# Kernel optimization log

Hardware: AMD Instinct MI355X
Metric: run time of the kernel (lower is better)

## Reference

```python
import jax, jax.numpy as jnp
import numpy as np

GROUP_SIZE = 128

def setup_inputs() -> dict:
    key = jax.random.key(0)
    k1, k2, k3 = jax.random.split(key, 3)
    B, S, K, N = 4, 128, 4096, 11008
    num_groups = K // GROUP_SIZE
    x = jax.random.normal(k1, (B, S, K), dtype=jnp.float16)
    # packed int4 weights: each byte holds two nibbles (low = even k, high = odd k)
    weight_packed = jax.random.randint(k2, (N, K // 2), 0, 256, dtype=jnp.int32)
    scales = (jax.random.uniform(k3, (N, num_groups), dtype=jnp.float16) * jnp.float16(0.1))
    return {"x": x, "weight_packed": weight_packed, "scales": scales}

def reference(x, weight_packed, scales):
    # x: (B, S, K) fp16; weight_packed: (N, K//2) int in [0,256); scales: (N, K//group_size) fp16
    N, Kp = weight_packed.shape
    K = Kp * 2
    # Unpack nibbles: even k -> low nibble, odd k -> high nibble (interleaved along K)
    low = weight_packed & 0x0F
    high = (weight_packed >> 4) & 0x0F
    w_int = jnp.stack([low, high], axis=-1).reshape(N, K).astype(jnp.float32)  # (N, K)
    # Per-group dequantization: w = scale * (q - 8)
    scale_full = jnp.repeat(scales.astype(jnp.float32), GROUP_SIZE, axis=1)    # (N, K)
    w = scale_full * (w_int - 8.0)
    # fp32 accumulation, fp16 output (matches kernel: float accum, half store)
    y = jnp.einsum('bsk,nk->bsn', x.astype(jnp.float32), w)
    return y.astype(jnp.float16)
```

## Files before the change

### kernel.cpp

```cpp
#include <hip/hip_runtime.h>


typedef __attribute__((ext_vector_type(8)))  short short8;
typedef __attribute__((ext_vector_type(16))) float f32x16;
typedef __attribute__((ext_vector_type(4)))  float f32x4;
typedef __attribute__((ext_vector_type(4)))  int   i32x4;
typedef __attribute__((ext_vector_type(2)))  int   i32x2;

#define M_DIM 512
#define N_DIM 11008
#define K_DIM 4096
#define BM 256
#define BN 128
#define BK 64
#define KSPLIT 4
#define PAD 8
#define THREADS 256
#define NTILE_M (M_DIM / BM)
#define NTILE_N (N_DIM / BN)
#define NTILES  (NTILE_M * NTILE_N)
#define TILE_ELEMS (BM * BN)

#if defined(__has_builtin)
#  if __has_builtin(__builtin_amdgcn_cvt_pk_bf16_f32)
#    define HAVE_PK_BF16 1
#  endif
#endif
#ifndef HAVE_PK_BF16
#  define HAVE_PK_BF16 0
#endif

__device__ __forceinline__ unsigned int fbits(float f) {
    union { float f; unsigned int u; } c; c.f = f; return c.u;
}
__device__ __forceinline__ int pack2bf(float lo, float hi) {
#if HAVE_PK_BF16
    typedef __attribute__((ext_vector_type(2))) __bf16 bf16x2;
    bf16x2 p = __builtin_amdgcn_cvt_pk_bf16_f32(lo, hi);
    int r; __builtin_memcpy(&r, &p, 4);
    return r;
#else
    unsigned int ul = fbits(lo), uh = fbits(hi);
    unsigned int l = (ul + 0x7FFFu + ((ul >> 16) & 1u)) >> 16;
    unsigned int h = (uh + 0x7FFFu + ((uh >> 16) & 1u)) & 0xFFFF0000u;
    return (int)(h | l);
#endif
}

__global__ __launch_bounds__(THREADS)
void cvt_x(const float* __restrict__ x, unsigned short* __restrict__ xw)
{
    int idx = (blockIdx.x * THREADS + threadIdx.x) * 4;
    f32x4 v = *(const f32x4*)(x + idx);
    i32x2 p;
    p[0] = pack2bf(v[0], v[1]);
    p[1] = pack2bf(v[2], v[3]);
    *(i32x2*)(xw + idx) = p;
}

template<int KS, bool PRECVT>
__global__ __launch_bounds__(THREADS, 2)
void dq_gemm(const unsigned short* __restrict__ xw,
             const float* __restrict__ xf,
             const int* __restrict__ wp,
             const float* __restrict__ scales,
             float* __restrict__ out,
             float* __restrict__ partials)
{
    __shared__ __align__(16) unsigned short sA[BM][BK + PAD];
    __shared__ __align__(16) unsigned short sB[BN][BK + PAD];

    const int t  = threadIdx.x;
    const int bx = blockIdx.x;

    int m_idx, nb, ksp;
    if (KS == 4) {
        m_idx = (bx >> 3) & 1;
        int rest = (bx & 7) | ((bx >> 4) << 3);
        ksp = rest & 3;
        nb  = rest >> 2;
    } else {
        m_idx = bx & 1;
        nb  = bx >> 1;
        ksp = 0;
    }
    const int m0 = m_idx * BM;
    const int n0 = nb * BN;
    const int k0 = ksp * (K_DIM / KS);
    const int KITERS = (K_DIM / KS) / BK;

    const int wave = t >> 6;
    const int lane = t & 63;
    const int wm = (wave & 1) * 128;
    const int wn = (wave >> 1) * 64;
    const int lr = lane & 31;
    const int lk = (lane >> 5) * 8;

    f32x16 acc[4][2] = {};

    for (int kk = 0; kk < KITERS; ++kk) {
        const int kb = k0 + kk * BK;
        const int g  = kb >> 7;

        if constexpr (PRECVT) {
            #pragma unroll
            for (int i = 0; i < 8; ++i) {
                int c = i * 256 + t, row = c >> 3, col = (c & 7) * 8;
                *(i32x4*)&sA[row][col] =
                    *(const i32x4*)(xw + (size_t)(m0 + row) * K_DIM + kb + col);
            }
        } else {
            #pragma unroll
            for (int i = 0; i < 16; ++i) {
                int c = i * 256 + t, row = c >> 4, col = (c & 15) * 4;
                f32x4 v = *(const f32x4*)(xf + (size_t)(m0 + row) * K_DIM + kb + col);
                i32x2 p;
                p[0] = pack2bf(v[0], v[1]);
                p[1] = pack2bf(v[2], v[3]);
                *(i32x2*)&sA[row][col] = p;
            }
        }

        #pragma unroll
        for (int i = 0; i < 4; ++i) {
            int c = i * 256 + t, row = c >> 3, ic = (c & 7) * 4;
            i32x4 pv = *(const i32x4*)(wp + (size_t)(n0 + row) * (K_DIM / 2) + (kb >> 1) + ic);
            float s  = scales[(size_t)(n0 + row) * (K_DIM / 128) + g];
            float ns8 = s * -8.0f;
            i32x4 res;
            #pragma unroll
            for (int e = 0; e < 4; ++e) {
                int b = pv[e];
                res[e] = pack2bf((float)(b & 15) * s + ns8,
                                 (float)((b >> 4) & 15) * s + ns8);
            }
            *(i32x4*)&sB[row][ic * 2] = res;
        }

        __syncthreads();

        #pragma unroll
        for (int ks = 0; ks < BK; ks += 16) {
            short8 a[4], b[2];
            #pragma unroll
            for (int i = 0; i < 4; ++i)
                a[i] = *(const short8*)&sA[wm + i * 32 + lr][ks + lk];
            #pragma unroll
            for (int j = 0; j < 2; ++j)
                b[j] = *(const short8*)&sB[wn + j * 32 + lr][ks + lk];
            #pragma unroll
            for (int i = 0; i < 4; ++i)
                #pragma unroll
                for (int j = 0; j < 2; ++j)
                    acc[i][j] = __builtin_amdgcn_mfma_f32_32x32x16_bf16(
                        a[i], b[j], acc[i][j], 0, 0, 0);
        }

        __syncthreads();
    }

    const int rbase = (lane >> 5) * 4;
    if constexpr (KS == 1) {
        #pragma unroll
        for (int i = 0; i < 4; ++i) {
            int mg0 = m0 + wm + i * 32 + rbase;
            #pragma unroll
            for (int j = 0; j < 2; ++j) {
                int ng = n0 + wn + j * 32 + lr;
                #pragma unroll
                for (int r = 0; r < 16; ++r)
                    out[(size_t)(mg0 + (r & 3) + 8 * (r >> 2)) * N_DIM + ng] = acc[i][j][r];
            }
        }
    } else {
        float* my = partials + ((size_t)(m_idx * NTILE_N + nb) * KS + ksp) * TILE_ELEMS;
        #pragma unroll
        for (int i = 0; i < 4; ++i)
            #pragma unroll
            for (int j = 0; j < 2; ++j)
                #pragma unroll
                for (int q = 0; q < 4; ++q) {
                    int c = (i * 2 + j) * 4 + q;
                    f32x4 v;
                    v[0] = acc[i][j][q * 4 + 0];
                    v[1] = acc[i][j][q * 4 + 1];
                    v[2] = acc[i][j][q * 4 + 2];
                    v[3] = acc[i][j][q * 4 + 3];
                    *(f32x4*)(my + c * 1024 + t * 4) = v;
                }
    }
}

__global__ __launch_bounds__(THREADS)
void reduce_k(const float* __restrict__ partials, float* __restrict__ out)
{
    __shared__ float sT[128][132];

    const int b    = blockIdx.x;
    const int tile = b >> 1;
    const int h    = b & 1;
    const int m_idx = tile / NTILE_N;
    const int nb    = tile % NTILE_N;
    const int m0 = m_idx * BM + h * 128;
    const int n0 = nb * BN;
    const int u  = threadIdx.x;

    const float* base = partials + (size_t)tile * KSPLIT * TILE_ELEMS;

    #pragma unroll
    for (int it = 0; it < 16; ++it) {
        int idx = it * 256 + u;
        int c   = idx >> 7;
        int tl  = idx & 127;
        int t   = (tl & 63) | (h << 6) | ((tl & 64) << 1);
        int off = c * 1024 + t * 4;
        f32x4 s = *(const f32x4*)(base + off);
        s += *(const f32x4*)(base + TILE_ELEMS + off);
        s += *(const f32x4*)(base + 2 * TILE_ELEMS + off);
        s += *(const f32x4*)(base + 3 * TILE_ELEMS + off);
        int i = c >> 3, j = (c >> 2) & 1, q = c & 3;
        int lane = t & 63, wave = t >> 6;
        int mrow = i * 32 + (lane >> 5) * 4 + 8 * q;
        int ncol = (wave >> 1) * 64 + j * 32 + (lane & 31);
        sT[mrow + 0][ncol] = s[0];
        sT[mrow + 1][ncol] = s[1];
        sT[mrow + 2][ncol] = s[2];
        sT[mrow + 3][ncol] = s[3];
    }
    __syncthreads();

    #pragma unroll
    for (int it = 0; it < 16; ++it) {
        int idx = it * 256 + u;
        int row = idx >> 5;
        int c4  = (idx & 31) * 4;
        f32x4 v = *(const f32x4*)&sT[row][c4];
        *(f32x4*)(out + (size_t)(m0 + row) * N_DIM + n0 + c4) = v;
    }
}

extern "C" void kernel_launch(void* const* d_in, const int* in_sizes, int n_in,
                              void* d_out, int out_size, void* d_ws, size_t ws_size,
                              hipStream_t stream) {
    (void)in_sizes; (void)n_in; (void)out_size;
    const float* x      = (const float*)d_in[0];
    const int*   wpck   = (const int*)d_in[1];
    const float* scales = (const float*)d_in[2];
    float*       out    = (float*)d_out;

    const size_t XW_BYTES   = (size_t)M_DIM * K_DIM * 2;
    const size_t PART_OFF   = XW_BYTES;
    const size_t PART_BYTES = (size_t)NTILES * KSPLIT * TILE_ELEMS * 4;

    if (ws_size >= PART_OFF + PART_BYTES) {
        unsigned short* xw  = (unsigned short*)d_ws;
        float* part = (float*)((char*)d_ws + PART_OFF);
        cvt_x<<<(M_DIM * K_DIM) / (THREADS * 4), THREADS, 0, stream>>>(x, xw);
        dq_gemm<KSPLIT, true><<<NTILES * KSPLIT, THREADS, 0, stream>>>(
            xw, x, wpck, scales, out, part);
        reduce_k<<<NTILES * 2, THREADS, 0, stream>>>(part, out);
    } else if (ws_size >= XW_BYTES) {
        unsigned short* xw = (unsigned short*)d_ws;
        cvt_x<<<(M_DIM * K_DIM) / (THREADS * 4), THREADS, 0, stream>>>(x, xw);
        dq_gemm<1, true><<<NTILES, THREADS, 0, stream>>>(
            xw, x, wpck, scales, out, nullptr);
    } else {
        dq_gemm<1, false><<<NTILES, THREADS, 0, stream>>>(
            nullptr, x, wpck, scales, out, nullptr);
    }
}
```

Measured before the change: 221.1 us.

## Pre-dequantize weights to bf16 and run plain bf16 GEMM with async LDS loads

Replaces the split-K fused dequant GEMM plus reduction with three steps: a separate kernel that dequantizes the whole int4 weight matrix into a bf16 workspace, then a plain bf16 GEMM over 128x128 tiles using 16x16x32 MFMA, XOR-swizzled shared memory, and global_load_lds direct-to-LDS copies. The aim is to take dequant arithmetic out of the GEMM inner loop and drop the partials write/read and the reduction kernel. In exchange it writes and reads back about 90 MB of bf16 weights instead of reading packed int4 directly, and it depends on the workspace being large enough. The GEMM has no double buffering, so loads and MFMA are not overlapped.

```diff
diff --git a/kernel.cpp b/kernel.cpp
--- a/kernel.cpp
+++ b/kernel.cpp
@@ -2,32 +2,33 @@
 
 
 typedef __attribute__((ext_vector_type(8)))  short short8;
-typedef __attribute__((ext_vector_type(16))) float f32x16;
 typedef __attribute__((ext_vector_type(4)))  float f32x4;
 typedef __attribute__((ext_vector_type(4)))  int   i32x4;
 typedef __attribute__((ext_vector_type(2)))  int   i32x2;
+typedef unsigned int   u32;
+typedef unsigned short u16;
 
 #define M_DIM 512
 #define N_DIM 11008
 #define K_DIM 4096
-#define BM 256
+#define BM 128
 #define BN 128
 #define BK 64
-#define KSPLIT 4
-#define PAD 8
 #define THREADS 256
-#define NTILE_M (M_DIM / BM)
-#define NTILE_N (N_DIM / BN)
-#define NTILES  (NTILE_M * NTILE_N)
-#define TILE_ELEMS (BM * BN)
 
 #if defined(__has_builtin)
 #  if __has_builtin(__builtin_amdgcn_cvt_pk_bf16_f32)
 #    define HAVE_PK_BF16 1
 #  endif
+#  if __has_builtin(__builtin_amdgcn_global_load_lds)
+#    define HAVE_GLLDS 1
+#  endif
 #endif
 #ifndef HAVE_PK_BF16
 #  define HAVE_PK_BF16 0
+#endif
+#ifndef HAVE_GLLDS
+#  define HAVE_GLLDS 0
 #endif
 
 __device__ __forceinline__ unsigned int fbits(float f) {
@@ -47,8 +48,16 @@
 #endif
 }
 
+__device__ __forceinline__ void async16(const u16* g, u16* lds_wave_base) {
+#if HAVE_GLLDS
+    __builtin_amdgcn_global_load_lds(
+        (const __attribute__((address_space(1))) u32*)g,
+        (__attribute__((address_space(3))) u32*)lds_wave_base, 16, 0, 0);
+#endif
+}
+
 __global__ __launch_bounds__(THREADS)
-void cvt_x(const float* __restrict__ x, unsigned short* __restrict__ xw)
+void cvt_x(const float* __restrict__ x, u16* __restrict__ xw)
 {
     int idx = (blockIdx.x * THREADS + threadIdx.x) * 4;
     f32x4 v = *(const f32x4*)(x + idx);
@@ -58,50 +67,139 @@
     *(i32x2*)(xw + idx) = p;
 }
 
-template<int KS, bool PRECVT>
+__global__ __launch_bounds__(THREADS)
+void dq_w(const int* __restrict__ wp, const float* __restrict__ scales,
+          u16* __restrict__ wb)
+{
+    size_t ci = (size_t)blockIdx.x * THREADS + threadIdx.x;
+    int n  = (int)(ci >> 9);
+    int jc = (int)(ci & 511);
+    float s   = scales[n * 32 + (jc >> 4)];
+    float ns8 = s * -8.0f;
+    i32x4 pv = *(const i32x4*)(wp + ci * 4);
+    i32x4 res;
+    #pragma unroll
+    for (int e = 0; e < 4; ++e) {
+        int b = pv[e];
+        res[e] = pack2bf((float)(b & 15) * s + ns8,
+                         (float)((b >> 4) & 15) * s + ns8);
+    }
+    *(i32x4*)(wb + ci * 8) = res;
+}
+
 __global__ __launch_bounds__(THREADS, 2)
-void dq_gemm(const unsigned short* __restrict__ xw,
-             const float* __restrict__ xf,
-             const int* __restrict__ wp,
-             const float* __restrict__ scales,
-             float* __restrict__ out,
-             float* __restrict__ partials)
-{
-    __shared__ __align__(16) unsigned short sA[BM][BK + PAD];
-    __shared__ __align__(16) unsigned short sB[BN][BK + PAD];
+void gemm_bf16(const u16* __restrict__ A,
+               const u16* __restrict__ B,
+               float* __restrict__ out)
+{
+    __shared__ __align__(16) u16 sA[BM * BK];
+    __shared__ __align__(16) u16 sB[BN * BK];
+
+    const int t    = threadIdx.x;
+    const int lane = t & 63;
+    const int wave = t >> 6;
+    const int m0 = blockIdx.x * BM;
+    const int n0 = blockIdx.y * BN;
+
+    const int wm = (wave & 1) * 64;
+    const int wn = (wave >> 1) * 64;
+    const int lm   = lane & 15;
+    const int quad = lane >> 4;
+
+    f32x4 acc[4][4] = {};
+
+    for (int kb = 0; kb < K_DIM; kb += BK) {
+#if HAVE_GLLDS
+        #pragma unroll
+        for (int i = 0; i < 4; ++i) {
+            int ci  = i * 256 + t;
+            int row = ci >> 3;
+            int kc  = (ci & 7) ^ (row & 7);
+            u16* lb = sA + (size_t)(i * 256 + (t >> 6) * 64) * 8;
+            async16(A + (size_t)(m0 + row) * K_DIM + kb + kc * 8, lb);
+        }
+        #pragma unroll
+        for (int i = 0; i < 4; ++i) {
+            int ci  = i * 256 + t;
+            int row = ci >> 3;
+            int kc  = (ci & 7) ^ (row & 7);
+            u16* lb = sB + (size_t)(i * 256 + (t >> 6) * 64) * 8;
+            async16(B + (size_t)(n0 + row) * K_DIM + kb + kc * 8, lb);
+        }
+#else
+        #pragma unroll
+        for (int i = 0; i < 4; ++i) {
+            int ci  = i * 256 + t;
+            int row = ci >> 3;
+            int kc  = (ci & 7) ^ (row & 7);
+            *(i32x4*)(sA + (size_t)ci * 8) =
+                *(const i32x4*)(A + (size_t)(m0 + row) * K_DIM + kb + kc * 8);
+            *(i32x4*)(sB + (size_t)ci * 8) =
+                *(const i32x4*)(B + (size_t)(n0 + row) * K_DIM + kb + kc * 8);
+        }
+#endif
+        __syncthreads();
+
+        #pragma unroll
+        for (int ks = 0; ks < BK; ks += 32) {
+            const int kc = (ks >> 3) + quad;
+            short8 a[4], b[4];
+            #pragma unroll
+            for (int i = 0; i < 4; ++i) {
+                int row = wm + i * 16 + lm;
+                a[i] = *(const short8*)&sA[(row * 8 + (kc ^ (row & 7))) * 8];
+            }
+            #pragma unroll
+            for (int j = 0; j < 4; ++j) {
+                int row = wn + j * 16 + lm;
+                b[j] = *(const short8*)&sB[(row * 8 + (kc ^ (row & 7))) * 8];
+            }
+            #pragma unroll
+            for (int i = 0; i < 4; ++i)
+                #pragma unroll
+                for (int j = 0; j < 4; ++j)
+                    acc[i][j] = __builtin_amdgcn_mfma_f32_16x16x32_bf16(
+                        a[i], b[j], acc[i][j], 0, 0, 0);
+        }
+
+        __syncthreads();
+    }
+
+    #pragma unroll
+    for (int i = 0; i < 4; ++i) {
+        int mg = m0 + wm + i * 16 + quad * 4;
+        #pragma unroll
+        for (int j = 0; j < 4; ++j) {
+            int ng = n0 + wn + j * 16 + lm;
+            #pragma unroll
+            for (int r = 0; r < 4; ++r)
+                out[(size_t)(mg + r) * N_DIM + ng] = acc[i][j][r];
+        }
+    }
+}
+
+#define PAD 8
+template<bool PRECVT>
+__global__ __launch_bounds__(THREADS, 2)
+void dq_gemm_fb(const u16* __restrict__ xw, const float* __restrict__ xf,
+                const int* __restrict__ wp, const float* __restrict__ scales,
+                float* __restrict__ out)
+{
+    __shared__ __align__(16) u16 sA[256][BK + PAD];
+    __shared__ __align__(16) u16 sB[128][BK + PAD];
+    typedef __attribute__((ext_vector_type(16))) float f32x16;
 
     const int t  = threadIdx.x;
-    const int bx = blockIdx.x;
-
-    int m_idx, nb, ksp;
-    if (KS == 4) {
-        m_idx = (bx >> 3) & 1;
-        int rest = (bx & 7) | ((bx >> 4) << 3);
-        ksp = rest & 3;
-        nb  = rest >> 2;
-    } else {
-        m_idx = bx & 1;
-        nb  = bx >> 1;
-        ksp = 0;
-    }
-    const int m0 = m_idx * BM;
-    const int n0 = nb * BN;
-    const int k0 = ksp * (K_DIM / KS);
-    const int KITERS = (K_DIM / KS) / BK;
-
-    const int wave = t >> 6;
-    const int lane = t & 63;
-    const int wm = (wave & 1) * 128;
-    const int wn = (wave >> 1) * 64;
-    const int lr = lane & 31;
-    const int lk = (lane >> 5) * 8;
+    const int m_idx = blockIdx.x & 1, nb = blockIdx.x >> 1;
+    const int m0 = m_idx * 256, n0 = nb * 128;
+    const int wave = t >> 6, lane = t & 63;
+    const int wm = (wave & 1) * 128, wn = (wave >> 1) * 64;
+    const int lr = lane & 31, lk = (lane >> 5) * 8;
 
     f32x16 acc[4][2] = {};
 
-    for (int kk = 0; kk < KITERS; ++kk) {
-        const int kb = k0 + kk * BK;
-        const int g  = kb >> 7;
-
+    for (int kb = 0; kb < K_DIM; kb += BK) {
+        const int g = kb >> 7;
         if constexpr (PRECVT) {
             #pragma unroll
             for (int i = 0; i < 8; ++i) {
@@ -120,12 +218,11 @@
                 *(i32x2*)&sA[row][col] = p;
             }
         }
-
         #pragma unroll
         for (int i = 0; i < 4; ++i) {
             int c = i * 256 + t, row = c >> 3, ic = (c & 7) * 4;
             i32x4 pv = *(const i32x4*)(wp + (size_t)(n0 + row) * (K_DIM / 2) + (kb >> 1) + ic);
-            float s  = scales[(size_t)(n0 + row) * (K_DIM / 128) + g];
+            float s  = scales[(size_t)(n0 + row) * 32 + g];
             float ns8 = s * -8.0f;
             i32x4 res;
             #pragma unroll
@@ -136,9 +233,7 @@
             }
             *(i32x4*)&sB[row][ic * 2] = res;
         }
-
-        __syncthreads();
-
+        __syncthreads();
         #pragma unroll
         for (int ks = 0; ks < BK; ks += 16) {
             short8 a[4], b[2];
@@ -155,87 +250,19 @@
                     acc[i][j] = __builtin_amdgcn_mfma_f32_32x32x16_bf16(
                         a[i], b[j], acc[i][j], 0, 0, 0);
         }
-
-        __syncthreads();
-    }
-
+        __syncthreads();
+    }
     const int rbase = (lane >> 5) * 4;
-    if constexpr (KS == 1) {
-        #pragma unroll
-        for (int i = 0; i < 4; ++i) {
-            int mg0 = m0 + wm + i * 32 + rbase;
-            #pragma unroll
-            for (int j = 0; j < 2; ++j) {
-                int ng = n0 + wn + j * 32 + lr;
-                #pragma unroll
-                for (int r = 0; r < 16; ++r)
-                    out[(size_t)(mg0 + (r & 3) + 8 * (r >> 2)) * N_DIM + ng] = acc[i][j][r];
-            }
-        }
-    } else {
-        float* my = partials + ((size_t)(m_idx * NTILE_N + nb) * KS + ksp) * TILE_ELEMS;
-        #pragma unroll
-        for (int i = 0; i < 4; ++i)
-            #pragma unroll
-            for (int j = 0; j < 2; ++j)
-                #pragma unroll
-                for (int q = 0; q < 4; ++q) {
-                    int c = (i * 2 + j) * 4 + q;
-                    f32x4 v;
-                    v[0] = acc[i][j][q * 4 + 0];
-                    v[1] = acc[i][j][q * 4 + 1];
-                    v[2] = acc[i][j][q * 4 + 2];
-                    v[3] = acc[i][j][q * 4 + 3];
-                    *(f32x4*)(my + c * 1024 + t * 4) = v;
-                }
-    }
-}
-
-__global__ __launch_bounds__(THREADS)
-void reduce_k(const float* __restrict__ partials, float* __restrict__ out)
-{
-    __shared__ float sT[128][132];
-
-    const int b    = blockIdx.x;
-    const int tile = b >> 1;
-    const int h    = b & 1;
-    const int m_idx = tile / NTILE_N;
-    const int nb    = tile % NTILE_N;
-    const int m0 = m_idx * BM + h * 128;
-    const int n0 = nb * BN;
-    const int u  = threadIdx.x;
-
-    const float* base = partials + (size_t)tile * KSPLIT * TILE_ELEMS;
-
     #pragma unroll
-    for (int it = 0; it < 16; ++it) {
-        int idx = it * 256 + u;
-        int c   = idx >> 7;
-        int tl  = idx & 127;
-        int t   = (tl & 63) | (h << 6) | ((tl & 64) << 1);
-        int off = c * 1024 + t * 4;
-        f32x4 s = *(const f32x4*)(base + off);
-        s += *(const f32x4*)(base + TILE_ELEMS + off);
-        s += *(const f32x4*)(base + 2 * TILE_ELEMS + off);
-        s += *(const f32x4*)(base + 3 * TILE_ELEMS + off);
-        int i = c >> 3, j = (c >> 2) & 1, q = c & 3;
-        int lane = t & 63, wave = t >> 6;
-        int mrow = i * 32 + (lane >> 5) * 4 + 8 * q;
-        int ncol = (wave >> 1) * 64 + j * 32 + (lane & 31);
-        sT[mrow + 0][ncol] = s[0];
-        sT[mrow + 1][ncol] = s[1];
-        sT[mrow + 2][ncol] = s[2];
-        sT[mrow + 3][ncol] = s[3];
-    }
-    __syncthreads();
-
-    #pragma unroll
-    for (int it = 0; it < 16; ++it) {
-        int idx = it * 256 + u;
-        int row = idx >> 5;
-        int c4  = (idx & 31) * 4;
-        f32x4 v = *(const f32x4*)&sT[row][c4];
-        *(f32x4*)(out + (size_t)(m0 + row) * N_DIM + n0 + c4) = v;
+    for (int i = 0; i < 4; ++i) {
+        int mg0 = m0 + wm + i * 32 + rbase;
+        #pragma unroll
+        for (int j = 0; j < 2; ++j) {
+            int ng = n0 + wn + j * 32 + lr;
+            #pragma unroll
+            for (int r = 0; r < 16; ++r)
+                out[(size_t)(mg0 + (r & 3) + 8 * (r >> 2)) * N_DIM + ng] = acc[i][j][r];
+        }
     }
 }
 
@@ -248,24 +275,23 @@
     const float* scales = (const float*)d_in[2];
     float*       out    = (float*)d_out;
 
-    const size_t XW_BYTES   = (size_t)M_DIM * K_DIM * 2;
-    const size_t PART_OFF   = XW_BYTES;
-    const size_t PART_BYTES = (size_t)NTILES * KSPLIT * TILE_ELEMS * 4;
-
-    if (ws_size >= PART_OFF + PART_BYTES) {
-        unsigned short* xw  = (unsigned short*)d_ws;
-        float* part = (float*)((char*)d_ws + PART_OFF);
+    const size_t XW_BYTES = (size_t)M_DIM * K_DIM * 2;
+    const size_t WB_OFF   = XW_BYTES;
+    const size_t WB_BYTES = (size_t)N_DIM * K_DIM * 2;
+
+    if (ws_size >= WB_OFF + WB_BYTES) {
+        u16* xw = (u16*)d_ws;
+        u16* wb = (u16*)((char*)d_ws + WB_OFF);
         cvt_x<<<(M_DIM * K_DIM) / (THREADS * 4), THREADS, 0, stream>>>(x, xw);
-        dq_gemm<KSPLIT, true><<<NTILES * KSPLIT, THREADS, 0, stream>>>(
-            xw, x, wpck, scales, out, part);
-        reduce_k<<<NTILES * 2, THREADS, 0, stream>>>(part, out);
+        dq_w<<<(int)(((size_t)N_DIM * K_DIM / 8) / THREADS), THREADS, 0, stream>>>(
+            wpck, scales, wb);
+        dim3 grid(M_DIM / BM, N_DIM / BN);
+        gemm_bf16<<<grid, dim3(THREADS), 0, stream>>>(xw, wb, out);
     } else if (ws_size >= XW_BYTES) {
-        unsigned short* xw = (unsigned short*)d_ws;
+        u16* xw = (u16*)d_ws;
         cvt_x<<<(M_DIM * K_DIM) / (THREADS * 4), THREADS, 0, stream>>>(x, xw);
-        dq_gemm<1, true><<<NTILES, THREADS, 0, stream>>>(
-            xw, x, wpck, scales, out, nullptr);
+        dq_gemm_fb<true><<<2 * 86, THREADS, 0, stream>>>(xw, x, wpck, scales, out);
     } else {
-        dq_gemm<1, false><<<NTILES, THREADS, 0, stream>>>(
-            nullptr, x, wpck, scales, out, nullptr);
-    }
-}
+        dq_gemm_fb<false><<<2 * 86, THREADS, 0, stream>>>(nullptr, x, wpck, scales, out);
+    }
+}
```

After: 248.5 us. 1.12x slower.

## Shrink M tile, swizzle LDS, use 16x16x32 MFMA and async A loads

Applied to the files above, without the earlier changes.

Halves the block M tile from 256 to 128, so there are twice as many GEMM blocks and smaller partial tiles for the split-K reduction. Padded LDS arrays are replaced by an XOR-swizzled layout, and the MFMA shape moves from 32x32x16 to 16x16x32 bf16. Activation tiles are loaded with global_load_lds direct-to-LDS when the builtin is available, and weight and scale loads are issued before the A loads. The aim is better occupancy and fewer LDS bank conflicts and register copies. The cost is that each weight tile is now dequantized and read from global memory by twice as many blocks.

```diff
diff --git a/kernel.cpp b/kernel.cpp
--- a/kernel.cpp
+++ b/kernel.cpp
@@ -2,32 +2,38 @@
 
 
 typedef __attribute__((ext_vector_type(8)))  short short8;
-typedef __attribute__((ext_vector_type(16))) float f32x16;
 typedef __attribute__((ext_vector_type(4)))  float f32x4;
 typedef __attribute__((ext_vector_type(4)))  int   i32x4;
 typedef __attribute__((ext_vector_type(2)))  int   i32x2;
+typedef unsigned int   u32;
+typedef unsigned short u16;
 
 #define M_DIM 512
 #define N_DIM 11008
 #define K_DIM 4096
-#define BM 256
+#define BM 128
 #define BN 128
 #define BK 64
 #define KSPLIT 4
-#define PAD 8
 #define THREADS 256
-#define NTILE_M (M_DIM / BM)
-#define NTILE_N (N_DIM / BN)
+#define NTILE_M 4
+#define NTILE_N 86
 #define NTILES  (NTILE_M * NTILE_N)
-#define TILE_ELEMS (BM * BN)
+#define TILE_EL (BM * BN)
 
 #if defined(__has_builtin)
 #  if __has_builtin(__builtin_amdgcn_cvt_pk_bf16_f32)
 #    define HAVE_PK_BF16 1
 #  endif
+#  if __has_builtin(__builtin_amdgcn_global_load_lds)
+#    define HAVE_GLLDS 1
+#  endif
 #endif
 #ifndef HAVE_PK_BF16
 #  define HAVE_PK_BF16 0
+#endif
+#ifndef HAVE_GLLDS
+#  define HAVE_GLLDS 0
 #endif
 
 __device__ __forceinline__ unsigned int fbits(float f) {
@@ -47,8 +53,16 @@
 #endif
 }
 
+__device__ __forceinline__ void async16(const u16* g, u16* lds) {
+#if HAVE_GLLDS
+    __builtin_amdgcn_global_load_lds(
+        (const __attribute__((address_space(1))) u32*)g,
+        (__attribute__((address_space(3))) u32*)lds, 16, 0, 0);
+#endif
+}
+
 __global__ __launch_bounds__(THREADS)
-void cvt_x(const float* __restrict__ x, unsigned short* __restrict__ xw)
+void cvt_x(const float* __restrict__ x, u16* __restrict__ xw)
 {
     int idx = (blockIdx.x * THREADS + threadIdx.x) * 4;
     f32x4 v = *(const f32x4*)(x + idx);
@@ -60,28 +74,28 @@
 
 template<int KS, bool PRECVT>
 __global__ __launch_bounds__(THREADS, 2)
-void dq_gemm(const unsigned short* __restrict__ xw,
-             const float* __restrict__ xf,
-             const int* __restrict__ wp,
-             const float* __restrict__ scales,
-             float* __restrict__ out,
-             float* __restrict__ partials)
+void dq_gemm(const u16* __restrict__ xw, const float* __restrict__ xf,
+             const int* __restrict__ wp, const float* __restrict__ scales,
+             float* __restrict__ out, float* __restrict__ partials)
 {
-    __shared__ __align__(16) unsigned short sA[BM][BK + PAD];
-    __shared__ __align__(16) unsigned short sB[BN][BK + PAD];
-
-    const int t  = threadIdx.x;
-    const int bx = blockIdx.x;
+    __shared__ __align__(16) u16 sA[BM * BK];
+    __shared__ __align__(16) u16 sB[BN * BK];
+
+    const int t    = threadIdx.x;
+    const int lane = t & 63;
+    const int wave = t >> 6;
+    const int bx   = blockIdx.x;
 
     int m_idx, nb, ksp;
     if (KS == 4) {
-        m_idx = (bx >> 3) & 1;
-        int rest = (bx & 7) | ((bx >> 4) << 3);
-        ksp = rest & 3;
-        nb  = rest >> 2;
+        int x = bx & 7, s = bx >> 3;
+        m_idx = s & 3;
+        int q = (s >> 2) * 8 + x;
+        ksp = q & 3;
+        nb  = q >> 2;
     } else {
-        m_idx = bx & 1;
-        nb  = bx >> 1;
+        m_idx = bx & 3;
+        nb  = bx >> 2;
         ksp = 0;
     }
     const int m0 = m_idx * BM;
@@ -89,139 +103,154 @@
     const int k0 = ksp * (K_DIM / KS);
     const int KITERS = (K_DIM / KS) / BK;
 
-    const int wave = t >> 6;
-    const int lane = t & 63;
-    const int wm = (wave & 1) * 128;
+    const int wm = (wave & 1) * 64;
     const int wn = (wave >> 1) * 64;
-    const int lr = lane & 31;
-    const int lk = (lane >> 5) * 8;
-
-    f32x16 acc[4][2] = {};
+    const int lm   = lane & 15;
+    const int quad = lane >> 4;
+
+    f32x4 acc[4][4] = {};
 
     for (int kk = 0; kk < KITERS; ++kk) {
         const int kb = k0 + kk * BK;
         const int g  = kb >> 7;
 
+        i32x4 pv[4];
+        float sc[4];
+        #pragma unroll
+        for (int i = 0; i < 4; ++i) {
+            int ci = i * 256 + t, row = ci >> 3;
+            int kcg = (ci & 7) ^ (row & 7);
+            pv[i] = *(const i32x4*)(wp + (size_t)(n0 + row) * (K_DIM / 2) + (kb >> 1) + kcg * 4);
+            sc[i] = scales[(size_t)(n0 + row) * 32 + g];
+        }
+
         if constexpr (PRECVT) {
+#if HAVE_GLLDS
+            #pragma unroll
+            for (int i = 0; i < 4; ++i) {
+                int ci = i * 256 + t, row = ci >> 3;
+                int kcg = (ci & 7) ^ (row & 7);
+                u16* lb = sA + (size_t)(i * 256 + wave * 64) * 8;
+                async16(xw + (size_t)(m0 + row) * K_DIM + kb + kcg * 8, lb);
+            }
+#else
+            #pragma unroll
+            for (int i = 0; i < 4; ++i) {
+                int ci = i * 256 + t, row = ci >> 3;
+                int kcg = (ci & 7) ^ (row & 7);
+                *(i32x4*)(sA + (size_t)ci * 8) =
+                    *(const i32x4*)(xw + (size_t)(m0 + row) * K_DIM + kb + kcg * 8);
+            }
+#endif
+        } else {
             #pragma unroll
             for (int i = 0; i < 8; ++i) {
-                int c = i * 256 + t, row = c >> 3, col = (c & 7) * 8;
-                *(i32x4*)&sA[row][col] =
-                    *(const i32x4*)(xw + (size_t)(m0 + row) * K_DIM + kb + col);
-            }
-        } else {
-            #pragma unroll
-            for (int i = 0; i < 16; ++i) {
-                int c = i * 256 + t, row = c >> 4, col = (c & 15) * 4;
-                f32x4 v = *(const f32x4*)(xf + (size_t)(m0 + row) * K_DIM + kb + col);
+                int c = i * 256 + t;
+                int row = c >> 4;
+                int col4 = (c & 15) * 4;
+                int kc = col4 >> 3, half = (col4 >> 2) & 1;
+                f32x4 v = *(const f32x4*)(xf + (size_t)(m0 + row) * K_DIM + kb + col4);
                 i32x2 p;
                 p[0] = pack2bf(v[0], v[1]);
                 p[1] = pack2bf(v[2], v[3]);
-                *(i32x2*)&sA[row][col] = p;
+                *(i32x2*)(sA + (size_t)(row * 8 + (kc ^ (row & 7))) * 8 + half * 4) = p;
             }
         }
 
         #pragma unroll
         for (int i = 0; i < 4; ++i) {
-            int c = i * 256 + t, row = c >> 3, ic = (c & 7) * 4;
-            i32x4 pv = *(const i32x4*)(wp + (size_t)(n0 + row) * (K_DIM / 2) + (kb >> 1) + ic);
-            float s  = scales[(size_t)(n0 + row) * (K_DIM / 128) + g];
-            float ns8 = s * -8.0f;
+            int ci = i * 256 + t;
+            float s = sc[i], ns8 = s * -8.0f;
             i32x4 res;
             #pragma unroll
             for (int e = 0; e < 4; ++e) {
-                int b = pv[e];
+                int b = pv[i][e];
                 res[e] = pack2bf((float)(b & 15) * s + ns8,
                                  (float)((b >> 4) & 15) * s + ns8);
             }
-            *(i32x4*)&sB[row][ic * 2] = res;
+            *(i32x4*)(sB + (size_t)ci * 8) = res;
         }
 
         __syncthreads();
 
         #pragma unroll
-        for (int ks = 0; ks < BK; ks += 16) {
-            short8 a[4], b[2];
-            #pragma unroll
-            for (int i = 0; i < 4; ++i)
-                a[i] = *(const short8*)&sA[wm + i * 32 + lr][ks + lk];
-            #pragma unroll
-            for (int j = 0; j < 2; ++j)
-                b[j] = *(const short8*)&sB[wn + j * 32 + lr][ks + lk];
+        for (int ks = 0; ks < BK; ks += 32) {
+            const int kc = (ks >> 3) + quad;
+            short8 a[4], b[4];
+            #pragma unroll
+            for (int i = 0; i < 4; ++i) {
+                int row = wm + i * 16 + lm;
+                a[i] = *(const short8*)&sA[(row * 8 + (kc ^ (row & 7))) * 8];
+            }
+            #pragma unroll
+            for (int j = 0; j < 4; ++j) {
+                int row = wn + j * 16 + lm;
+                b[j] = *(const short8*)&sB[(row * 8 + (kc ^ (row & 7))) * 8];
+            }
             #pragma unroll
             for (int i = 0; i < 4; ++i)
                 #pragma unroll
-                for (int j = 0; j < 2; ++j)
-                    acc[i][j] = __builtin_amdgcn_mfma_f32_32x32x16_bf16(
+                for (int j = 0; j < 4; ++j)
+                    acc[i][j] = __builtin_amdgcn_mfma_f32_16x16x32_bf16(
                         a[i], b[j], acc[i][j], 0, 0, 0);
         }
 
         __syncthreads();
     }
 
-    const int rbase = (lane >> 5) * 4;
     if constexpr (KS == 1) {
         #pragma unroll
         for (int i = 0; i < 4; ++i) {
-            int mg0 = m0 + wm + i * 32 + rbase;
-            #pragma unroll
-            for (int j = 0; j < 2; ++j) {
-                int ng = n0 + wn + j * 32 + lr;
+            int mg = m0 + wm + i * 16 + quad * 4;
+            #pragma unroll
+            for (int j = 0; j < 4; ++j) {
+                int ng = n0 + wn + j * 16 + lm;
                 #pragma unroll
-                for (int r = 0; r < 16; ++r)
-                    out[(size_t)(mg0 + (r & 3) + 8 * (r >> 2)) * N_DIM + ng] = acc[i][j][r];
+                for (int r = 0; r < 4; ++r)
+                    out[(size_t)(mg + r) * N_DIM + ng] = acc[i][j][r];
             }
         }
     } else {
-        float* my = partials + ((size_t)(m_idx * NTILE_N + nb) * KS + ksp) * TILE_ELEMS;
+        float* my = partials + ((size_t)(m_idx * NTILE_N + nb) * KS + ksp) * TILE_EL;
         #pragma unroll
         for (int i = 0; i < 4; ++i)
             #pragma unroll
-            for (int j = 0; j < 2; ++j)
-                #pragma unroll
-                for (int q = 0; q < 4; ++q) {
-                    int c = (i * 2 + j) * 4 + q;
-                    f32x4 v;
-                    v[0] = acc[i][j][q * 4 + 0];
-                    v[1] = acc[i][j][q * 4 + 1];
-                    v[2] = acc[i][j][q * 4 + 2];
-                    v[3] = acc[i][j][q * 4 + 3];
-                    *(f32x4*)(my + c * 1024 + t * 4) = v;
-                }
+            for (int j = 0; j < 4; ++j)
+                *(f32x4*)(my + (i * 4 + j) * 1024 + t * 4) = acc[i][j];
     }
 }
 
 __global__ __launch_bounds__(THREADS)
 void reduce_k(const float* __restrict__ partials, float* __restrict__ out)
 {
-    __shared__ float sT[128][132];
+    __shared__ float sT[64][132];
 
     const int b    = blockIdx.x;
     const int tile = b >> 1;
     const int h    = b & 1;
     const int m_idx = tile / NTILE_N;
     const int nb    = tile % NTILE_N;
-    const int m0 = m_idx * BM + h * 128;
+    const int m0 = m_idx * BM + h * 64;
     const int n0 = nb * BN;
     const int u  = threadIdx.x;
 
-    const float* base = partials + (size_t)tile * KSPLIT * TILE_ELEMS;
+    const float* base = partials + (size_t)tile * KSPLIT * TILE_EL;
 
     #pragma unroll
-    for (int it = 0; it < 16; ++it) {
+    for (int it = 0; it < 8; ++it) {
         int idx = it * 256 + u;
         int c   = idx >> 7;
         int tl  = idx & 127;
-        int t   = (tl & 63) | (h << 6) | ((tl & 64) << 1);
+        int t   = (tl & 63) | (h << 6) | ((tl >> 6) << 7);
         int off = c * 1024 + t * 4;
         f32x4 s = *(const f32x4*)(base + off);
-        s += *(const f32x4*)(base + TILE_ELEMS + off);
-        s += *(const f32x4*)(base + 2 * TILE_ELEMS + off);
-        s += *(const f32x4*)(base + 3 * TILE_ELEMS + off);
-        int i = c >> 3, j = (c >> 2) & 1, q = c & 3;
+        s += *(const f32x4*)(base + TILE_EL + off);
+        s += *(const f32x4*)(base + 2 * TILE_EL + off);
+        s += *(const f32x4*)(base + 3 * TILE_EL + off);
+        int i = c >> 2, j = c & 3;
         int lane = t & 63, wave = t >> 6;
-        int mrow = i * 32 + (lane >> 5) * 4 + 8 * q;
-        int ncol = (wave >> 1) * 64 + j * 32 + (lane & 31);
+        int mrow = i * 16 + (lane >> 4) * 4;
+        int ncol = (wave >> 1) * 64 + j * 16 + (lane & 15);
         sT[mrow + 0][ncol] = s[0];
         sT[mrow + 1][ncol] = s[1];
         sT[mrow + 2][ncol] = s[2];
@@ -230,7 +259,7 @@
     __syncthreads();
 
     #pragma unroll
-    for (int it = 0; it < 16; ++it) {
+    for (int it = 0; it < 8; ++it) {
         int idx = it * 256 + u;
         int row = idx >> 5;
         int c4  = (idx & 31) * 4;
@@ -250,17 +279,17 @@
 
     const size_t XW_BYTES   = (size_t)M_DIM * K_DIM * 2;
     const size_t PART_OFF   = XW_BYTES;
-    const size_t PART_BYTES = (size_t)NTILES * KSPLIT * TILE_ELEMS * 4;
+    const size_t PART_BYTES = (size_t)NTILES * KSPLIT * TILE_EL * 4;
 
     if (ws_size >= PART_OFF + PART_BYTES) {
-        unsigned short* xw  = (unsigned short*)d_ws;
+        u16*   xw   = (u16*)d_ws;
         float* part = (float*)((char*)d_ws + PART_OFF);
         cvt_x<<<(M_DIM * K_DIM) / (THREADS * 4), THREADS, 0, stream>>>(x, xw);
         dq_gemm<KSPLIT, true><<<NTILES * KSPLIT, THREADS, 0, stream>>>(
             xw, x, wpck, scales, out, part);
         reduce_k<<<NTILES * 2, THREADS, 0, stream>>>(part, out);
     } else if (ws_size >= XW_BYTES) {
-        unsigned short* xw = (unsigned short*)d_ws;
+        u16* xw = (u16*)d_ws;
         cvt_x<<<(M_DIM * K_DIM) / (THREADS * 4), THREADS, 0, stream>>>(x, xw);
         dq_gemm<1, true><<<NTILES, THREADS, 0, stream>>>(
             xw, x, wpck, scales, out, nullptr);
```

Measured after the change: 223.4 us. About the same (+1.1%).
